# Kernel optimization log

Hardware: AMD Instinct MI355X
Metric: run time of the kernel (lower is better)

The kernel has to match this reference:

```python
import jax, jax.numpy as jnp
import numpy as np

B, T, C, HEAD = 4, 4096, 1024, 64
SCALE = 1.0 / (C ** 0.5)  # module divides by embedding_size**0.5, not head_size**0.5


def setup_inputs() -> dict:
    key = jax.random.key(0)
    kx, kq, kk, kv = jax.random.split(key, 4)
    x = jax.random.normal(kx, (B, T, C), dtype=jnp.float32)
    # nn.Linear(C, head_size, bias=False) weights, stored as (C, head_size) for x @ W
    Wq = jax.random.normal(kq, (C, HEAD), dtype=jnp.float32) * (1.0 / np.sqrt(C))
    Wk = jax.random.normal(kk, (C, HEAD), dtype=jnp.float32) * (1.0 / np.sqrt(C))
    Wv = jax.random.normal(kv, (C, HEAD), dtype=jnp.float32) * (1.0 / np.sqrt(C))
    return {"x": x, "Wq": Wq, "Wk": Wk, "Wv": Wv}


def reference(x, Wq, Wk, Wv):
    q = jnp.einsum('btc,ch->bth', x, Wq)  # [B,T,HEAD]
    k = jnp.einsum('btc,ch->bth', x, Wk)
    v = jnp.einsum('btc,ch->bth', x, Wv)
    aff = jnp.einsum('bqh,bkh->bqk', q, k) * SCALE  # [B,T,T]
    causal = jnp.tril(jnp.ones((T, T), dtype=bool))
    aff = jnp.where(causal, aff, -jnp.inf)
    p = jax.nn.softmax(aff, axis=-1)  # dropout p=0.0 -> identity
    return jnp.einsum('bqk,bkh->bqh', p, v)  # [B,T,HEAD]
```

## Files before the change

### kernel.cpp

```cpp
#include <hip/hip_runtime.h>

#define T_SEQ 4096
#define NBATCH 4
#define CDIM 1024
#define NHEAD 64
#define SCALE (1.0f / 32.0f)
#define LOG2E 1.4426950408889634f
#define BT (NBATCH * T_SEQ)
#define NW 8
#define WREG 8960

typedef __bf16 bf16x8 __attribute__((ext_vector_type(8)));
typedef float f32x4 __attribute__((ext_vector_type(4)));
typedef float f32x16 __attribute__((ext_vector_type(16)));

__device__ __forceinline__ unsigned short f2bf(float f) {
  union { float f; unsigned u; } x;
  x.f = f;
  unsigned r = x.u + 0x7FFFu + ((x.u >> 16) & 1u);
  return (unsigned short)(r >> 16);
}

__device__ __forceinline__ unsigned cvt_pk(float lo, float hi) {
  unsigned d;
  asm("v_cvt_pk_bf16_f32 %0, %1, %2" : "=v"(d) : "v"(lo), "v"(hi));
  return d;
}

__device__ __forceinline__ void swap32(unsigned& a, unsigned& b) {
  asm("v_permlane32_swap_b32 %0, %1" : "+v"(a), "+v"(b));
}

__device__ __forceinline__ f32x4 mfma16(bf16x8 a, bf16x8 b, f32x4 c) {
  return __builtin_amdgcn_mfma_f32_16x16x32_bf16(a, b, c, 0, 0, 0);
}

__device__ __forceinline__ f32x16 mfma32(bf16x8 a, bf16x8 b, f32x16 c) {
  return __builtin_amdgcn_mfma_f32_32x32x16_bf16(a, b, c, 0, 0, 0);
}

__global__ __launch_bounds__(256) void prep_w(
    const float* __restrict__ Wq, const float* __restrict__ Wk,
    const float* __restrict__ Wv, unsigned short* __restrict__ Wt) {
  __shared__ float wlds[64][65];
  const int m = blockIdx.x / 16;
  const int kt = blockIdx.x % 16;
  const float* W = (m == 0) ? Wq : (m == 1) ? Wk : Wv;
  const float s = (m == 0) ? (SCALE * LOG2E) : 1.0f;
  const int tid = threadIdx.x;
  const int la = tid & 63;
  const int gr = tid >> 6;

  for (int i = 0; i < 16; i++) {
    int kl = gr * 16 + i;
    wlds[kl][la] = W[(size_t)(kt * 64 + kl) * NHEAD + la];
  }
  __syncthreads();
  for (int i = 0; i < 16; i++) {
    int cl = gr * 16 + i;
    Wt[(size_t)(m * 64 + cl) * CDIM + kt * 64 + la] = f2bf(wlds[la][cl] * s);
  }
}

__global__ __launch_bounds__(256) void proj_qkv(
    const float* __restrict__ x, const unsigned short* __restrict__ Wt,
    unsigned short* __restrict__ qws, unsigned short* __restrict__ kws,
    unsigned short* __restrict__ vtws) {
  __shared__ unsigned short xlds[2][32][136];
  const int tid = threadIdx.x;
  const int lane = tid & 63;
  const int w = tid >> 6;
  const int g = lane >> 4;
  const int c15 = lane & 15;
  const int rb = blockIdx.x * 32;

  f32x4 acc[2][3];
  for (int i = 0; i < 2; i++)
    for (int j = 0; j < 3; j++) acc[i][j] = (f32x4){0.f, 0.f, 0.f, 0.f};

  const int sr = tid >> 3;
  const int scc = (tid & 7) * 16;
  const float* xrow = x + (size_t)(rb + sr) * CDIM + scc;

  {
    float4 cur[4];
    for (int i = 0; i < 4; i++) cur[i] = *(const float4*)(xrow + i * 4);
    unsigned short pk[16];
    for (int i = 0; i < 4; i++) {
      pk[i * 4 + 0] = f2bf(cur[i].x);
      pk[i * 4 + 1] = f2bf(cur[i].y);
      pk[i * 4 + 2] = f2bf(cur[i].z);
      pk[i * 4 + 3] = f2bf(cur[i].w);
    }
    *(bf16x8*)&xlds[0][sr][scc] = *(bf16x8*)&pk[0];
    *(bf16x8*)&xlds[0][sr][scc + 8] = *(bf16x8*)&pk[8];
  }
  __syncthreads();

  int pb = 0;
  for (int k0 = 0; k0 < CDIM; k0 += 128) {
    const bool more = (k0 + 128 < CDIM);
    float4 nxt[4];
    if (more)
      for (int i = 0; i < 4; i++)
        nxt[i] = *(const float4*)(xrow + k0 + 128 + i * 4);

    bf16x8 wfrag[4][3];
    for (int kk = 0; kk < 4; kk++)
      for (int bn = 0; bn < 3; bn++) {
        int col = w * 48 + bn * 16 + c15;
        wfrag[kk][bn] =
            *(const bf16x8*)&Wt[(size_t)col * CDIM + k0 + kk * 32 + g * 8];
      }

    for (int kk = 0; kk < 4; kk++) {
      bf16x8 a[2];
      for (int mt = 0; mt < 2; mt++)
        a[mt] = *(bf16x8*)&xlds[pb][mt * 16 + c15][kk * 32 + g * 8];
      for (int bn = 0; bn < 3; bn++)
        for (int mt = 0; mt < 2; mt++)
          acc[mt][bn] = mfma16(a[mt], wfrag[kk][bn], acc[mt][bn]);
    }

    if (more) {
      unsigned short pk[16];
      for (int i = 0; i < 4; i++) {
        pk[i * 4 + 0] = f2bf(nxt[i].x);
        pk[i * 4 + 1] = f2bf(nxt[i].y);
        pk[i * 4 + 2] = f2bf(nxt[i].z);
        pk[i * 4 + 3] = f2bf(nxt[i].w);
      }
      *(bf16x8*)&xlds[pb ^ 1][sr][scc] = *(bf16x8*)&pk[0];
      *(bf16x8*)&xlds[pb ^ 1][sr][scc + 8] = *(bf16x8*)&pk[8];
    }
    __syncthreads();
    pb ^= 1;
  }

  for (int mt = 0; mt < 2; mt++)
    for (int bn = 0; bn < 3; bn++) {
      int col = w * 48 + bn * 16 + c15;
      int row0 = rb + mt * 16 + 4 * g;
      for (int r = 0; r < 4; r++) {
        unsigned short v = f2bf(acc[mt][bn][r]);
        int t = row0 + r;
        if (col < 64)
          qws[(size_t)t * 64 + col] = v;
        else if (col < 128)
          kws[(size_t)t * 64 + (col - 64)] = v;
        else
          vtws[(size_t)(col - 128) * BT + t] = v;
      }
    }
}

__global__ __launch_bounds__(512, 2) void attn_fwd(
    const unsigned short* __restrict__ qws, const unsigned short* __restrict__ kws,
    const unsigned short* __restrict__ vtws, float* __restrict__ out) {
  __shared__ __align__(16) char smem[NW * WREG];
  const int tid = threadIdx.x;
  const int lane = tid & 63;
  const int w = tid >> 6;
  const int q31 = lane & 31;
  const int hi = lane >> 5;
  const int b = blockIdx.x >> 6;
  const int pi = blockIdx.x & 63;
  const size_t rowbase = (size_t)b * T_SEQ;
  char* wbase = smem + w * WREG;

  for (int half = 0; half < 2; ++half) {
    const int qt = half ? (127 - pi) : pi;
    const int qb = qt * 32;
    const int nsteps = qt + 1;

    bf16x8 qf[4];
    for (int h2 = 0; h2 < 4; h2++)
      qf[h2] = *(const bf16x8*)&qws[(rowbase + qb + q31) * 64 + h2 * 16 + hi * 8];

    f32x16 o[2];
    o[0] = (f32x16)0.f;
    o[1] = (f32x16)0.f;
    float mrow = -1e30f;
    float lrun = 0.f;

    for (int st = w; st < nsteps; st += NW) {
      const int kt = st * 32;
      bf16x8 ka[4];
      for (int h2 = 0; h2 < 4; h2++)
        ka[h2] =
            *(const bf16x8*)&kws[(rowbase + kt + q31) * 64 + h2 * 16 + hi * 8];
      bf16x8 va[2][2];
      for (int nt = 0; nt < 2; nt++)
        for (int ki = 0; ki < 2; ki++)
          va[nt][ki] = *(const bf16x8*)&vtws[(size_t)(nt * 32 + q31) * BT +
                                             rowbase + kt + ki * 16 + hi * 8];

      f32x16 s = (f32x16)0.f;
      for (int h2 = 0; h2 < 4; h2++) s = mfma32(ka[h2], qf[h2], s);

      float sv[16];
      for (int r = 0; r < 16; r++) sv[r] = s[r];

      if (st == nsteps - 1) {
        for (int r = 0; r < 16; r++) {
          int key = kt + (r & 3) + 8 * (r >> 2) + 4 * hi;
          if (key > qb + q31) sv[r] = -1e30f;
        }
      }

      float t01 = fmaxf(sv[0], sv[1]), t23 = fmaxf(sv[2], sv[3]);
      float t45 = fmaxf(sv[4], sv[5]), t67 = fmaxf(sv[6], sv[7]);
      float t89 = fmaxf(sv[8], sv[9]), tab = fmaxf(sv[10], sv[11]);
      float tcd = fmaxf(sv[12], sv[13]), tef = fmaxf(sv[14], sv[15]);
      float t = fmaxf(fmaxf(fmaxf(t01, t23), fmaxf(t45, t67)),
                      fmaxf(fmaxf(t89, tab), fmaxf(tcd, tef)));
      t = fmaxf(t, __shfl_xor(t, 32));

      float mn = fmaxf(mrow, t);
      float a = exp2f(mrow - mn);
      mrow = mn;
      o[0] *= a;
      o[1] *= a;
      lrun *= a;

      float p[16];
      for (int r = 0; r < 16; r++) p[r] = exp2f(sv[r] - mrow);

      float ssum = 0.f;
      for (int r = 0; r < 16; r++) ssum += p[r];
      lrun += ssum + __shfl_xor(ssum, 32);

      unsigned X[8];
      for (int jj = 0; jj < 8; jj++) X[jj] = cvt_pk(p[2 * jj], p[2 * jj + 1]);
      swap32(X[0], X[2]);
      swap32(X[1], X[3]);
      swap32(X[4], X[6]);
      swap32(X[5], X[7]);

      union { unsigned u[4]; bf16x8 v; } bf0, bf1;
      bf0.u[0] = X[0]; bf0.u[1] = X[1]; bf0.u[2] = X[2]; bf0.u[3] = X[3];
      bf1.u[0] = X[4]; bf1.u[1] = X[5]; bf1.u[2] = X[6]; bf1.u[3] = X[7];

      for (int nt = 0; nt < 2; nt++) {
        o[nt] = mfma32(va[nt][0], bf0.v, o[nt]);
        o[nt] = mfma32(va[nt][1], bf1.v, o[nt]);
      }
    }

    float* ow = (float*)wbase;
    float* mw = (float*)(wbase + 8704);
    float* lw = (float*)(wbase + 8832);
    for (int nt = 0; nt < 2; nt++)
      for (int r = 0; r < 16; r++) {
        int d = nt * 32 + (r & 3) + 8 * (r >> 2) + 4 * hi;
        ow[q31 * 68 + d] = o[nt][r];
      }
    if (hi == 0) {
      mw[q31] = mrow;
      lw[q31] = lrun;
    }
    __syncthreads();

    for (int i = 0; i < 4; i++) {
      int e = tid + i * 512;
      int row = e >> 6;
      int d = e & 63;
      float M = -1e30f;
      for (int ww = 0; ww < NW; ww++)
        M = fmaxf(M, ((const float*)(smem + ww * WREG + 8704))[row]);
      float L = 0.f, O = 0.f;
      for (int ww = 0; ww < NW; ww++) {
        float mv = ((const float*)(smem + ww * WREG + 8704))[row];
        float f = exp2f(mv - M);
        L += f * ((const float*)(smem + ww * WREG + 8832))[row];
        O += f * ((const float*)(smem + ww * WREG))[row * 68 + d];
      }
      out[(rowbase + qb + row) * 64 + d] = O / L;
    }
    __syncthreads();
  }
}

extern "C" void kernel_launch(void* const* d_in, const int* in_sizes, int n_in,
                              void* d_out, int out_size, void* d_ws, size_t ws_size,
                              hipStream_t stream) {
  const float* x = (const float*)d_in[0];
  const float* Wq = (const float*)d_in[1];
  const float* Wk = (const float*)d_in[2];
  const float* Wv = (const float*)d_in[3];
  float* out = (float*)d_out;

  char* ws = (char*)d_ws;
  unsigned short* Wt = (unsigned short*)(ws);
  unsigned short* qws = (unsigned short*)(ws + 393216);
  unsigned short* kws = (unsigned short*)(ws + 393216 + 2097152);
  unsigned short* vtws = (unsigned short*)(ws + 393216 + 2 * 2097152);

  prep_w<<<dim3(48), dim3(256), 0, stream>>>(Wq, Wk, Wv, Wt);
  proj_qkv<<<dim3(512), dim3(256), 0, stream>>>(x, Wt, qws, kws, vtws);
  attn_fwd<<<dim3(256), dim3(512), 0, stream>>>(qws, kws, vtws, out);
}
```

Baseline: 79.77 us.

## Process both paired query tiles in one key loop to share K/V loads

The two query tiles each block handles (pi and 127-pi) used to be processed one after the other, each loading its own K and V fragments. They are now processed together in a single loop over key tiles: each K/V fragment is loaded once and applied to the long tile, and also to the short tile while its causal range still covers that key. This roughly halves global K/V traffic for the short tile's range and gives the scheduler more independent MFMA work per iteration. In exchange, each thread keeps two sets of Q fragments, accumulators and softmax state alive, which raises register pressure under launch_bounds(512,2) and could cause spills.

```diff
diff --git a/kernel.cpp b/kernel.cpp
--- a/kernel.cpp
+++ b/kernel.cpp
@@ -168,96 +168,107 @@
   const size_t rowbase = (size_t)b * T_SEQ;
   char* wbase = smem + w * WREG;
 
-  for (int half = 0; half < 2; ++half) {
-    const int qt = half ? (127 - pi) : pi;
-    const int qb = qt * 32;
-    const int nsteps = qt + 1;
-
-    bf16x8 qf[4];
+  const int qb0 = pi * 32;
+  const int qb1 = (127 - pi) * 32;
+  const int n0 = pi + 1;
+  const int n1 = 128 - pi;
+
+  bf16x8 qf0[4], qf1[4];
+  for (int h2 = 0; h2 < 4; h2++) {
+    qf0[h2] =
+        *(const bf16x8*)&qws[(rowbase + qb0 + q31) * 64 + h2 * 16 + hi * 8];
+    qf1[h2] =
+        *(const bf16x8*)&qws[(rowbase + qb1 + q31) * 64 + h2 * 16 + hi * 8];
+  }
+
+  f32x16 o0[2], o1[2];
+  o0[0] = (f32x16)0.f; o0[1] = (f32x16)0.f;
+  o1[0] = (f32x16)0.f; o1[1] = (f32x16)0.f;
+  float m0 = -1e30f, m1 = -1e30f;
+  float l0 = 0.f, l1 = 0.f;
+
+  auto STEP = [&](int st, int kt, int qb_, int nst, bf16x8 (&qf_)[4],
+                  f32x16 (&o_)[2], float& mrow_, float& lrun_,
+                  bf16x8 (&ka)[4], bf16x8 (&va)[2][2]) {
+    f32x16 s = (f32x16)0.f;
+    for (int h2 = 0; h2 < 4; h2++) s = mfma32(ka[h2], qf_[h2], s);
+
+    float sv[16];
+    for (int r = 0; r < 16; r++) sv[r] = s[r];
+    if (st == nst - 1) {
+      for (int r = 0; r < 16; r++) {
+        int key = kt + (r & 3) + 8 * (r >> 2) + 4 * hi;
+        if (key > qb_ + q31) sv[r] = -1e30f;
+      }
+    }
+
+    float t01 = fmaxf(sv[0], sv[1]), t23 = fmaxf(sv[2], sv[3]);
+    float t45 = fmaxf(sv[4], sv[5]), t67 = fmaxf(sv[6], sv[7]);
+    float t89 = fmaxf(sv[8], sv[9]), tab = fmaxf(sv[10], sv[11]);
+    float tcd = fmaxf(sv[12], sv[13]), tef = fmaxf(sv[14], sv[15]);
+    float t = fmaxf(fmaxf(fmaxf(t01, t23), fmaxf(t45, t67)),
+                    fmaxf(fmaxf(t89, tab), fmaxf(tcd, tef)));
+    t = fmaxf(t, __shfl_xor(t, 32));
+
+    float mn = fmaxf(mrow_, t);
+    float a = exp2f(mrow_ - mn);
+    mrow_ = mn;
+    o_[0] *= a;
+    o_[1] *= a;
+    lrun_ *= a;
+
+    float p[16];
+    for (int r = 0; r < 16; r++) p[r] = exp2f(sv[r] - mrow_);
+
+    float ssum = 0.f;
+    for (int r = 0; r < 16; r++) ssum += p[r];
+    lrun_ += ssum + __shfl_xor(ssum, 32);
+
+    unsigned X[8];
+    for (int jj = 0; jj < 8; jj++) X[jj] = cvt_pk(p[2 * jj], p[2 * jj + 1]);
+    swap32(X[0], X[2]);
+    swap32(X[1], X[3]);
+    swap32(X[4], X[6]);
+    swap32(X[5], X[7]);
+
+    union { unsigned u[4]; bf16x8 v; } bf0, bf1;
+    bf0.u[0] = X[0]; bf0.u[1] = X[1]; bf0.u[2] = X[2]; bf0.u[3] = X[3];
+    bf1.u[0] = X[4]; bf1.u[1] = X[5]; bf1.u[2] = X[6]; bf1.u[3] = X[7];
+
+    for (int nt = 0; nt < 2; nt++) {
+      o_[nt] = mfma32(va[nt][0], bf0.v, o_[nt]);
+      o_[nt] = mfma32(va[nt][1], bf1.v, o_[nt]);
+    }
+  };
+
+  for (int st = w; st < n1; st += NW) {
+    const int kt = st * 32;
+    bf16x8 ka[4];
     for (int h2 = 0; h2 < 4; h2++)
-      qf[h2] = *(const bf16x8*)&qws[(rowbase + qb + q31) * 64 + h2 * 16 + hi * 8];
-
-    f32x16 o[2];
-    o[0] = (f32x16)0.f;
-    o[1] = (f32x16)0.f;
-    float mrow = -1e30f;
-    float lrun = 0.f;
-
-    for (int st = w; st < nsteps; st += NW) {
-      const int kt = st * 32;
-      bf16x8 ka[4];
-      for (int h2 = 0; h2 < 4; h2++)
-        ka[h2] =
-            *(const bf16x8*)&kws[(rowbase + kt + q31) * 64 + h2 * 16 + hi * 8];
-      bf16x8 va[2][2];
-      for (int nt = 0; nt < 2; nt++)
-        for (int ki = 0; ki < 2; ki++)
-          va[nt][ki] = *(const bf16x8*)&vtws[(size_t)(nt * 32 + q31) * BT +
-                                             rowbase + kt + ki * 16 + hi * 8];
-
-      f32x16 s = (f32x16)0.f;
-      for (int h2 = 0; h2 < 4; h2++) s = mfma32(ka[h2], qf[h2], s);
-
-      float sv[16];
-      for (int r = 0; r < 16; r++) sv[r] = s[r];
-
-      if (st == nsteps - 1) {
-        for (int r = 0; r < 16; r++) {
-          int key = kt + (r & 3) + 8 * (r >> 2) + 4 * hi;
-          if (key > qb + q31) sv[r] = -1e30f;
-        }
-      }
-
-      float t01 = fmaxf(sv[0], sv[1]), t23 = fmaxf(sv[2], sv[3]);
-      float t45 = fmaxf(sv[4], sv[5]), t67 = fmaxf(sv[6], sv[7]);
-      float t89 = fmaxf(sv[8], sv[9]), tab = fmaxf(sv[10], sv[11]);
-      float tcd = fmaxf(sv[12], sv[13]), tef = fmaxf(sv[14], sv[15]);
-      float t = fmaxf(fmaxf(fmaxf(t01, t23), fmaxf(t45, t67)),
-                      fmaxf(fmaxf(t89, tab), fmaxf(tcd, tef)));
-      t = fmaxf(t, __shfl_xor(t, 32));
-
-      float mn = fmaxf(mrow, t);
-      float a = exp2f(mrow - mn);
-      mrow = mn;
-      o[0] *= a;
-      o[1] *= a;
-      lrun *= a;
-
-      float p[16];
-      for (int r = 0; r < 16; r++) p[r] = exp2f(sv[r] - mrow);
-
-      float ssum = 0.f;
-      for (int r = 0; r < 16; r++) ssum += p[r];
-      lrun += ssum + __shfl_xor(ssum, 32);
-
-      unsigned X[8];
-      for (int jj = 0; jj < 8; jj++) X[jj] = cvt_pk(p[2 * jj], p[2 * jj + 1]);
-      swap32(X[0], X[2]);
-      swap32(X[1], X[3]);
-      swap32(X[4], X[6]);
-      swap32(X[5], X[7]);
-
-      union { unsigned u[4]; bf16x8 v; } bf0, bf1;
-      bf0.u[0] = X[0]; bf0.u[1] = X[1]; bf0.u[2] = X[2]; bf0.u[3] = X[3];
-      bf1.u[0] = X[4]; bf1.u[1] = X[5]; bf1.u[2] = X[6]; bf1.u[3] = X[7];
-
-      for (int nt = 0; nt < 2; nt++) {
-        o[nt] = mfma32(va[nt][0], bf0.v, o[nt]);
-        o[nt] = mfma32(va[nt][1], bf1.v, o[nt]);
-      }
-    }
-
+      ka[h2] = *(const bf16x8*)&kws[(rowbase + kt + q31) * 64 + h2 * 16 + hi * 8];
+    bf16x8 va[2][2];
+    for (int nt = 0; nt < 2; nt++)
+      for (int ki = 0; ki < 2; ki++)
+        va[nt][ki] = *(const bf16x8*)&vtws[(size_t)(nt * 32 + q31) * BT +
+                                           rowbase + kt + ki * 16 + hi * 8];
+
+    STEP(st, kt, qb1, n1, qf1, o1, m1, l1, ka, va);
+    if (st < n0)
+      STEP(st, kt, qb0, n0, qf0, o0, m0, l0, ka, va);
+  }
+
+  auto EPI = [&](int qb_, f32x16 (&o_)[2], float mrow_, float lrun_) {
     float* ow = (float*)wbase;
     float* mw = (float*)(wbase + 8704);
     float* lw = (float*)(wbase + 8832);
     for (int nt = 0; nt < 2; nt++)
       for (int r = 0; r < 16; r++) {
         int d = nt * 32 + (r & 3) + 8 * (r >> 2) + 4 * hi;
-        ow[q31 * 68 + d] = o[nt][r];
+        ow[q31 * 68 + d] = o_[nt][r];
       }
     if (hi == 0) {
-      mw[q31] = mrow;
-      lw[q31] = lrun;
+      mw[q31] = mrow_;
+      lw[q31] = lrun_;
     }
     __syncthreads();
 
@@ -275,10 +286,12 @@
         L += f * ((const float*)(smem + ww * WREG + 8832))[row];
         O += f * ((const float*)(smem + ww * WREG))[row * 68 + d];
       }
-      out[(rowbase + qb + row) * 64 + d] = O / L;
+      out[(rowbase + qb_ + row) * 64 + d] = O / L;
     }
     __syncthreads();
-  }
+  };
+  EPI(qb1, o1, m1, l1);
+  EPI(qb0, o0, m0, l0);
 }
 
 extern "C" void kernel_launch(void* const* d_in, const int* in_sizes, int n_in,
```

After: 79.01 us, median of 4. Within noise of the previous version (-1.0%).
